# Optimization experiments

Measured on AMD Instinct MI355X. Metric: run time of the kernel, lower is better.

Reference implementation:

```python
import jax, jax.numpy as jnp
import numpy as np

M = 4        # num_modalities
C = 128      # in_channels
NH = 4       # num_heads
HD = C // NH # head_dim = 32
OUT = 128    # out_channels
B, D, H, W = 1, 12, 12, 12
N = D * H * W
EPS = 1e-5
SCALE = float(np.sqrt(HD))


def setup_inputs() -> dict:
    key = jax.random.key(0)
    ks = jax.random.split(key, 12)
    inp = {}
    for i in range(M):
        inp[f"feat{i}"] = jax.random.normal(ks[i], (B, C, D, H, W), dtype=jnp.float32)
    s = 1.0 / np.sqrt(C)
    inp["Wq"] = jax.random.normal(ks[4], (M, C, C), dtype=jnp.float32) * s
    inp["Wk"] = jax.random.normal(ks[5], (M, C, C), dtype=jnp.float32) * s
    inp["Wv"] = jax.random.normal(ks[6], (M, C, C), dtype=jnp.float32) * s
    inp["Wout"] = jax.random.normal(ks[7], (OUT, C), dtype=jnp.float32) * s
    inp["bn_gamma"] = jnp.ones((OUT,), jnp.float32)
    inp["bn_beta"] = jnp.zeros((OUT,), jnp.float32)
    inp["bn_mean"] = jax.random.normal(ks[8], (OUT,), dtype=jnp.float32) * 0.1
    inp["bn_var"] = jax.random.uniform(ks[9], (OUT,), dtype=jnp.float32, minval=0.5, maxval=1.5)
    return inp


def _proj(Wm, feats):
    # per-modality 1x1 conv == matmul over channels: [M,C,C] x [M,B,C,N] -> [M,B,nh,N,hd]
    p = jnp.einsum('moc,mbcn->mbon', Wm, feats)
    return p.reshape(M, B, NH, HD, N).transpose(0, 1, 2, 4, 3)


def reference(feat0, feat1, feat2, feat3, Wq, Wk, Wv, Wout,
              bn_gamma, bn_beta, bn_mean, bn_var):
    feats = jnp.stack([feat0, feat1, feat2, feat3]).reshape(M, B, C, N)
    Q = _proj(Wq, feats)   # [M,B,nh,N,hd]
    K = _proj(Wk, feats)
    V = _proj(Wv, feats)
    # concat K/V over modalities along token axis -> [B,nh,M*N,hd]
    Kall = K.transpose(1, 2, 0, 3, 4).reshape(B, NH, M * N, HD)
    Vall = V.transpose(1, 2, 0, 3, 4).reshape(B, NH, M * N, HD)
    fused = jnp.zeros((B, NH, N, HD), jnp.float32)
    for i in range(M):  # small fixed loop over modalities
        attn = jnp.einsum('bhqd,bhkd->bhqk', Q[i], Kall) / SCALE  # [B,nh,N,M*N]
        attn = jax.nn.softmax(attn, axis=-1)  # dropout is identity at eval
        fused = fused + jnp.einsum('bhqk,bhkd->bhqd', attn, Vall)
    fused = fused.transpose(0, 1, 3, 2).reshape(B, C, N)
    # out_proj: 1x1 Conv3d -> BN (eval, running stats) -> ReLU
    y = jnp.einsum('oc,bcn->bon', Wout, fused)
    inv = bn_gamma / jnp.sqrt(bn_var + EPS)
    y = y * inv[None, :, None] + (bn_beta - bn_mean * inv)[None, :, None]
    return jax.nn.relu(y).reshape(B, OUT, D, H, W)
```

## Files before the change

kernel.cpp:

```cpp
#include <hip/hip_runtime.h>

#define MODS 4
#define CH   128
#define NHD  4
#define HDIM 32
#define NTOK 1728
#define NG   (NTOK/4)
#define NKEY (MODS*NTOK)
#define NT   27
#define QSC (0.17677669529663687f * 1.4426950408889634f)

#ifndef __has_builtin
#define __has_builtin(x) 0
#endif
#if __has_builtin(__builtin_amdgcn_exp2f)
#define EXP2(x) __builtin_amdgcn_exp2f(x)
#else
#define EXP2(x) __expf(0.69314718055994531f * (x))
#endif

typedef __bf16 bf16x8 __attribute__((ext_vector_type(8)));
typedef float  f32x16 __attribute__((ext_vector_type(16)));

__device__ inline bf16x8 ldb8(const unsigned short* p) {
    return *reinterpret_cast<const bf16x8*>(p);
}
__device__ inline unsigned int pkbf(float a, float b) {
    unsigned short ua = __builtin_bit_cast(unsigned short, (__bf16)a);
    unsigned short ub = __builtin_bit_cast(unsigned short, (__bf16)b);
    return (unsigned int)ua | ((unsigned int)ub << 16);
}
__device__ inline void glds16(const unsigned short* g, unsigned short* l) {
    __builtin_amdgcn_global_load_lds(
        (const __attribute__((address_space(1))) unsigned int*)(g),
        (__attribute__((address_space(3))) unsigned int*)(l), 16, 0, 0);
}

__global__ __launch_bounds__(256) void proj_kernel(
    const float* __restrict__ f0, const float* __restrict__ f1,
    const float* __restrict__ f2, const float* __restrict__ f3,
    const float* __restrict__ Wq, const float* __restrict__ Wk,
    const float* __restrict__ Wv,
    unsigned short* __restrict__ Qb, unsigned short* __restrict__ Kb,
    unsigned short* __restrict__ V2)
{
    __shared__ __align__(16) float Wt[64][68];
    __shared__ __align__(16) float fs[64][68];

    const int tid = threadIdx.x;
    const int bid = blockIdx.x;
    const int tm  = bid / 54;
    const int rem = bid % 54;
    const int oh  = rem & 1;
    const int nt  = rem >> 1;
    const int t   = tm >> 2, m = tm & 3;
    const int nb  = nt * 64;

    const float* fsrc = (m == 0) ? f0 : (m == 1) ? f1 : (m == 2) ? f2 : f3;
    const float* W    = ((t == 0) ? Wq : (t == 1) ? Wk : Wv) + (size_t)m * CH * CH;

    const int o0 = (tid >> 4) * 4, nn0 = (tid & 15) * 4;
    float acc[4][4] = {};

    for (int ch = 0; ch < 2; ++ch) {
        if (ch) __syncthreads();
        {
            const int o = tid & 63, c4b = tid >> 6;
            #pragma unroll
            for (int j = 0; j < 4; ++j) {
                const int c4 = c4b + 4 * j;
                float4 wv = *reinterpret_cast<const float4*>(
                    W + (size_t)(oh * 64 + o) * CH + ch * 64 + c4 * 4);
                Wt[c4*4+0][o] = wv.x; Wt[c4*4+1][o] = wv.y;
                Wt[c4*4+2][o] = wv.z; Wt[c4*4+3][o] = wv.w;
            }
        }
        {
            const int nchunk = tid & 15, cb = tid >> 4;
            #pragma unroll
            for (int j = 0; j < 4; ++j) {
                const int c = cb + 16 * j;
                float4 v = *reinterpret_cast<const float4*>(
                    fsrc + (size_t)(ch * 64 + c) * NTOK + nb + nchunk * 4);
                *reinterpret_cast<float4*>(&fs[c][nchunk * 4]) = v;
            }
        }
        __syncthreads();
        #pragma unroll 4
        for (int c = 0; c < 64; ++c) {
            float4 wv = *reinterpret_cast<const float4*>(&Wt[c][o0]);
            float4 fv = *reinterpret_cast<const float4*>(&fs[c][nn0]);
            acc[0][0] = fmaf(wv.x, fv.x, acc[0][0]); acc[0][1] = fmaf(wv.x, fv.y, acc[0][1]);
            acc[0][2] = fmaf(wv.x, fv.z, acc[0][2]); acc[0][3] = fmaf(wv.x, fv.w, acc[0][3]);
            acc[1][0] = fmaf(wv.y, fv.x, acc[1][0]); acc[1][1] = fmaf(wv.y, fv.y, acc[1][1]);
            acc[1][2] = fmaf(wv.y, fv.z, acc[1][2]); acc[1][3] = fmaf(wv.y, fv.w, acc[1][3]);
            acc[2][0] = fmaf(wv.z, fv.x, acc[2][0]); acc[2][1] = fmaf(wv.z, fv.y, acc[2][1]);
            acc[2][2] = fmaf(wv.z, fv.z, acc[2][2]); acc[2][3] = fmaf(wv.z, fv.w, acc[2][3]);
            acc[3][0] = fmaf(wv.w, fv.x, acc[3][0]); acc[3][1] = fmaf(wv.w, fv.y, acc[3][1]);
            acc[3][2] = fmaf(wv.w, fv.z, acc[3][2]); acc[3][3] = fmaf(wv.w, fv.w, acc[3][3]);
        }
    }

    const int og0 = oh * 64 + o0;
    const int h = og0 >> 5, d0 = og0 & 31;
    const int ng = nb + nn0;
    if (t == 2) {
        const int off = ng & 15;
        const int ng2 = (ng & ~15) + ((off & 4) << 1) + ((off & 8) >> 1);
        #pragma unroll
        for (int i = 0; i < 4; ++i) {
            ushort4 pk;
            pk.x = __builtin_bit_cast(unsigned short, (__bf16)acc[i][0]);
            pk.y = __builtin_bit_cast(unsigned short, (__bf16)acc[i][1]);
            pk.z = __builtin_bit_cast(unsigned short, (__bf16)acc[i][2]);
            pk.w = __builtin_bit_cast(unsigned short, (__bf16)acc[i][3]);
            *reinterpret_cast<ushort4*>(V2 + (size_t)(h * HDIM + d0 + i) * NKEY + m * NTOK + ng2) = pk;
        }
    } else {
        const float sc = (t == 0) ? QSC : 1.0f;
        unsigned short* base = ((t == 0) ? Qb : Kb)
            + (((size_t)(m * NHD + h)) * NTOK + ng) * HDIM + d0;
        #pragma unroll
        for (int j = 0; j < 4; ++j) {
            unsigned short* row = base + (size_t)j * HDIM;
            *reinterpret_cast<unsigned int*>(row)     = pkbf(acc[0][j] * sc, acc[1][j] * sc);
            *reinterpret_cast<unsigned int*>(row + 2) = pkbf(acc[2][j] * sc, acc[3][j] * sc);
        }
    }
}

__global__ __launch_bounds__(256, 6) void attn_kernel(
    const unsigned short* __restrict__ Qb, const unsigned short* __restrict__ Kb,
    const unsigned short* __restrict__ V2,
    float* __restrict__ accT, float* __restrict__ sR)
{
    __shared__ __align__(16) unsigned short smAll[2][2][2][1024];

    const int tid  = threadIdx.x;
    const int lane = tid & 63;
    const int w    = tid >> 6;
    const int qslot = w & 1;
    const int ks    = w >> 1;
    const int l31  = lane & 31;
    const int hi   = lane >> 5;

    const int bid  = blockIdx.x;
    const int slot = bid & 7;
    const int h    = slot >> 1;
    const int ko   = slot & 1;
    const int rest = bid >> 3;
    const int qb   = rest % 108;
    const int kseg = rest / 108;
    const int qtile = qb * 2 + qslot;
    const int qg0  = qtile * 32;
    const int im   = qg0 / NTOK;
    const int n0   = qg0 % NTOK;
    const int km   = ko * 2 + ks;
    const int p    = kseg * 2 + ko;

    const unsigned short* qp = Qb + (((size_t)(im * NHD + h)) * NTOK + n0 + l31) * HDIM + hi * 8;
    const bf16x8 qf0 = ldb8(qp);
    const bf16x8 qf1 = ldb8(qp + 16);

    const int rk0 = qslot * 16 + (lane >> 2);
    const int ck0 = (lane & 3) ^ ((rk0 >> 1) & 3);
    const unsigned short* gk0 = Kb
        + (((size_t)(km * NHD + h)) * NTOK + kseg * 864 + rk0) * HDIM + ck0 * 8;
    const int dv0 = qslot * 16 + (lane >> 2);
    const int cv0 = (lane & 3) ^ (dv0 & 3);
    const unsigned short* gv0 = V2
        + ((size_t)(h * HDIM + dv0)) * NKEY + km * NTOK + kseg * 864 + cv0 * 8;

    const int fK = (l31 >> 1) & 3, fV = l31 & 3;
    const int kA0 = l31 * 32 + ((hi ^ fK) << 3);
    const int kB0 = l31 * 32 + (((2 + hi) ^ fK) << 3);
    const int vo0 = l31 * 32 + ((hi ^ fV) << 3);
    const int vo1 = l31 * 32 + (((2 + hi) ^ fV) << 3);

    f32x16 z;
    #pragma unroll
    for (int r = 0; r < 16; ++r) z[r] = 0.f;
    f32x16 o_acc = z, s_acc = z;
    bf16x8 onesv;
    #pragma unroll
    for (int j = 0; j < 8; ++j) onesv[j] = (__bf16)1.0f;

    #define STAGE(bb) do {                                      \
        glds16(gk0, &smAll[bb][ks][0][0] + qslot * 512);        \
        glds16(gv0, &smAll[bb][ks][1][0] + qslot * 512);        \
        gk0 += 1024; gv0 += 32;                                 \
    } while (0)

    STAGE(0);
    __syncthreads();

    int buf = 0;
    for (int t = 0; t < NT; ++t) {
        if (t + 1 < NT) STAGE(buf ^ 1);
        const unsigned short* Kl = &smAll[buf][ks][0][0];
        const unsigned short* Vl = &smAll[buf][ks][1][0];

        bf16x8 k0 = ldb8(Kl + kA0);
        bf16x8 k1 = ldb8(Kl + kB0);
        f32x16 c = __builtin_amdgcn_mfma_f32_32x32x16_bf16(k0, qf0, z, 0, 0, 0);
        c = __builtin_amdgcn_mfma_f32_32x32x16_bf16(k1, qf1, c, 0, 0, 0);

        float e[16];
        #pragma unroll
        for (int r = 0; r < 16; ++r) e[r] = EXP2(c[r]);
        bf16x8 pa0, pa1;
        #pragma unroll
        for (int j = 0; j < 8; ++j) { pa0[j] = (__bf16)e[j]; pa1[j] = (__bf16)e[8 + j]; }

        bf16x8 v0 = ldb8(Vl + vo0);
        bf16x8 v1 = ldb8(Vl + vo1);

        o_acc = __builtin_amdgcn_mfma_f32_32x32x16_bf16(pa0, v0, o_acc, 0, 0, 0);
        o_acc = __builtin_amdgcn_mfma_f32_32x32x16_bf16(pa1, v1, o_acc, 0, 0, 0);
        s_acc = __builtin_amdgcn_mfma_f32_32x32x16_bf16(pa0, onesv, s_acc, 0, 0, 0);
        s_acc = __builtin_amdgcn_mfma_f32_32x32x16_bf16(pa1, onesv, s_acc, 0, 0, 0);

        __syncthreads();
        buf ^= 1;
    }
    #undef STAGE

    float* accf = (float*)&smAll[0][0][0][0];
    if (ks == 1) {
        #pragma unroll
        for (int r = 0; r < 16; ++r) {
            const int qrow = (r & 3) + 8 * (r >> 2) + 4 * hi;
            accf[(qslot * 32 + qrow) * 33 + l31] = o_acc[r];
            if (l31 == 0) accf[(qslot * 32 + qrow) * 33 + 32] = s_acc[r];
        }
    }
    __syncthreads();
    if (ks == 0) {
        #pragma unroll
        for (int r = 0; r < 16; ++r) {
            const int qrow = (r & 3) + 8 * (r >> 2) + 4 * hi;
            accf[(qslot * 32 + qrow) * 33 + l31] += o_acc[r];
            if (l31 == 0) accf[(qslot * 32 + qrow) * 33 + 32] += s_acc[r];
        }
    }
    __syncthreads();
    {
        const int q  = tid & 63;
        const int dq = tid >> 6;
        #pragma unroll
        for (int j = 0; j < 8; ++j) {
            const int d = dq * 8 + j;
            accT[((size_t)((p * 4 + h) * HDIM + d)) * NKEY + (size_t)qb * 64 + q]
                = accf[q * 33 + d];
        }
        if (tid < 64)
            sR[((size_t)(p * 4 + h)) * NKEY + (size_t)qb * 64 + tid] = accf[tid * 33 + 32];
    }
}

__global__ __launch_bounds__(256) void norm_kernel(
    const float* __restrict__ accT, const float* __restrict__ sR,
    float* __restrict__ fused)
{
    const int idx = blockIdx.x * 256 + threadIdx.x;
    const int c = idx / NTOK;
    const int n = idx % NTOK;
    const int h = c >> 5, d = c & 31;
    float acc = 0.f;
    #pragma unroll
    for (int imq = 0; imq < MODS; ++imq) {
        const size_t q = (size_t)imq * NTOK + n;
        float s = 0.f, a = 0.f;
        #pragma unroll
        for (int pp = 0; pp < 4; ++pp) {
            s += sR[(size_t)(pp * 4 + h) * NKEY + q];
            a += accT[((size_t)((pp * 4 + h) * HDIM + d)) * NKEY + q];
        }
        acc = fmaf(a, 1.0f / s, acc);
    }
    fused[idx] = acc;
}

__global__ __launch_bounds__(256) void outproj_kernel(
    const float* __restrict__ fused, const float* __restrict__ Wout,
    const float* __restrict__ gamma, const float* __restrict__ beta,
    const float* __restrict__ mean,  const float* __restrict__ var,
    float* __restrict__ out)
{
    const int idx = blockIdx.x * 256 + threadIdx.x;
    const int n2 = idx % (NTOK / 2);
    const int o  = idx / (NTOK / 2);
    const float* W     = Wout + (size_t)o * CH;
    const float* fbase = fused + n2 * 2;
    float a0 = 0.f, a1 = 0.f;
    #pragma unroll 8
    for (int c = 0; c < CH; c += 4) {
        float4 w4 = *reinterpret_cast<const float4*>(W + c);
        float2 r0 = *reinterpret_cast<const float2*>(fbase + (size_t)(c + 0) * NTOK);
        float2 r1 = *reinterpret_cast<const float2*>(fbase + (size_t)(c + 1) * NTOK);
        float2 r2 = *reinterpret_cast<const float2*>(fbase + (size_t)(c + 2) * NTOK);
        float2 r3 = *reinterpret_cast<const float2*>(fbase + (size_t)(c + 3) * NTOK);
        a0 = fmaf(w4.x, r0.x, a0); a0 = fmaf(w4.y, r1.x, a0);
        a0 = fmaf(w4.z, r2.x, a0); a0 = fmaf(w4.w, r3.x, a0);
        a1 = fmaf(w4.x, r0.y, a1); a1 = fmaf(w4.y, r1.y, a1);
        a1 = fmaf(w4.z, r2.y, a1); a1 = fmaf(w4.w, r3.y, a1);
    }
    float inv = gamma[o] * rsqrtf(var[o] + 1e-5f);
    float sh  = fmaf(-mean[o], inv, beta[o]);
    float2 y;
    y.x = fmaxf(fmaf(a0, inv, sh), 0.f);
    y.y = fmaxf(fmaf(a1, inv, sh), 0.f);
    *reinterpret_cast<float2*>(out + (size_t)o * NTOK + n2 * 2) = y;
}

extern "C" void kernel_launch(void* const* d_in, const int* in_sizes, int n_in,
                              void* d_out, int out_size, void* d_ws, size_t ws_size,
                              hipStream_t stream)
{
    const float* f0    = (const float*)d_in[0];
    const float* f1    = (const float*)d_in[1];
    const float* f2    = (const float*)d_in[2];
    const float* f3    = (const float*)d_in[3];
    const float* Wq    = (const float*)d_in[4];
    const float* Wk    = (const float*)d_in[5];
    const float* Wv    = (const float*)d_in[6];
    const float* Wout  = (const float*)d_in[7];
    const float* gamma = (const float*)d_in[8];
    const float* beta  = (const float*)d_in[9];
    const float* mean  = (const float*)d_in[10];
    const float* var   = (const float*)d_in[11];
    float* out = (float*)d_out;

    const size_t QKV = (size_t)MODS * NHD * NTOK * HDIM;
    unsigned short* Qb = (unsigned short*)d_ws;
    unsigned short* Kb = Qb + QKV;
    unsigned short* V2 = Kb + QKV;
    float* accT  = (float*)(V2 + QKV);
    float* sR    = accT + (size_t)4 * NHD * HDIM * NKEY;
    float* fused = sR + (size_t)4 * NHD * NKEY;

    proj_kernel<<<648, 256, 0, stream>>>(f0, f1, f2, f3, Wq, Wk, Wv, Qb, Kb, V2);
    attn_kernel<<<1728, 256, 0, stream>>>(Qb, Kb, V2, accT, sR);
    norm_kernel<<<(CH * NTOK) / 256, 256, 0, stream>>>(accT, sR, fused);
    outproj_kernel<<<(CH * NTOK / 2) / 256, 256, 0, stream>>>(
        fused, Wout, gamma, beta, mean, var, out);
}
```

Baseline: 77.93 us.

## Use bf16 MFMA for QKV projection with a transposing bf16 prep kernel

Adds a prep kernel that converts features to bf16 in token-major layout and converts the Q/K/V weights to bf16, folding the query scale into Wq. The projection kernel then computes each 32-token by 128-output tile with 32x32x16 bf16 MFMA instructions instead of scalar fp32 FMAs. Results are staged through shared memory to write the Q/K and permuted V layouts. This cuts the projection's ALU cost, at the price of an extra kernel launch, extra workspace traffic, and bf16 rounding of the inputs.

```diff
diff --git a/kernel.cpp b/kernel.cpp
--- a/kernel.cpp
+++ b/kernel.cpp
@@ -5,7 +5,6 @@
 #define NHD  4
 #define HDIM 32
 #define NTOK 1728
-#define NG   (NTOK/4)
 #define NKEY (MODS*NTOK)
 #define NT   27
 #define QSC (0.17677669529663687f * 1.4426950408889634f)
@@ -25,10 +24,8 @@
 __device__ inline bf16x8 ldb8(const unsigned short* p) {
     return *reinterpret_cast<const bf16x8*>(p);
 }
-__device__ inline unsigned int pkbf(float a, float b) {
-    unsigned short ua = __builtin_bit_cast(unsigned short, (__bf16)a);
-    unsigned short ub = __builtin_bit_cast(unsigned short, (__bf16)b);
-    return (unsigned int)ua | ((unsigned int)ub << 16);
+__device__ inline unsigned short bfc(float x) {
+    return __builtin_bit_cast(unsigned short, (__bf16)x);
 }
 __device__ inline void glds16(const unsigned short* g, unsigned short* l) {
     __builtin_amdgcn_global_load_lds(
@@ -36,96 +33,125 @@
         (__attribute__((address_space(3))) unsigned int*)(l), 16, 0, 0);
 }
 
-__global__ __launch_bounds__(256) void proj_kernel(
+__global__ __launch_bounds__(256) void prep_kernel(
     const float* __restrict__ f0, const float* __restrict__ f1,
     const float* __restrict__ f2, const float* __restrict__ f3,
     const float* __restrict__ Wq, const float* __restrict__ Wk,
     const float* __restrict__ Wv,
+    unsigned short* __restrict__ fbT, unsigned short* __restrict__ Wb)
+{
+    const int tid = threadIdx.x;
+    const int bid = blockIdx.x;
+    if (bid < 216) {
+        __shared__ float tile[64][65];
+        const int m  = bid / 54;
+        const int r  = bid % 54;
+        const int cb = (r / 27) * 64;
+        const int nb = (r % 27) * 64;
+        const float* fsrc = (m == 0) ? f0 : (m == 1) ? f1 : (m == 2) ? f2 : f3;
+        const int n4 = tid & 15, cr = tid >> 4;
+        #pragma unroll
+        for (int j = 0; j < 4; ++j) {
+            const int c = cr + 16 * j;
+            float4 v = *reinterpret_cast<const float4*>(
+                fsrc + (size_t)(cb + c) * NTOK + nb + n4 * 4);
+            tile[c][n4*4+0] = v.x; tile[c][n4*4+1] = v.y;
+            tile[c][n4*4+2] = v.z; tile[c][n4*4+3] = v.w;
+        }
+        __syncthreads();
+        const int cq = tid & 15, nr0 = tid >> 4;
+        #pragma unroll
+        for (int j = 0; j < 4; ++j) {
+            const int nr = nr0 + 16 * j;
+            ushort4 pk;
+            pk.x = bfc(tile[cq*4+0][nr]); pk.y = bfc(tile[cq*4+1][nr]);
+            pk.z = bfc(tile[cq*4+2][nr]); pk.w = bfc(tile[cq*4+3][nr]);
+            *reinterpret_cast<ushort4*>(
+                fbT + ((size_t)m * NTOK + nb + nr) * CH + cb + cq * 4) = pk;
+        }
+    } else {
+        const int wb = bid - 216;
+        const size_t base = ((size_t)wb * 256 + tid) * 32;
+        #pragma unroll
+        for (int g = 0; g < 8; ++g) {
+            const size_t i = base + g * 4;
+            const int t = (int)(i >> 16);
+            const size_t off = i & 65535;
+            const float* W = (t == 0) ? Wq : (t == 1) ? Wk : Wv;
+            float4 v = *reinterpret_cast<const float4*>(W + off);
+            const float sc = (t == 0) ? QSC : 1.0f;
+            ushort4 pk;
+            pk.x = bfc(v.x * sc); pk.y = bfc(v.y * sc);
+            pk.z = bfc(v.z * sc); pk.w = bfc(v.w * sc);
+            *reinterpret_cast<ushort4*>(Wb + i) = pk;
+        }
+    }
+}
+
+__global__ __launch_bounds__(256) void proj_kernel(
+    const unsigned short* __restrict__ Wb, const unsigned short* __restrict__ fbT,
     unsigned short* __restrict__ Qb, unsigned short* __restrict__ Kb,
     unsigned short* __restrict__ V2)
 {
-    __shared__ __align__(16) float Wt[64][68];
-    __shared__ __align__(16) float fs[64][68];
+    __shared__ __align__(16) float accf[128 * 33];
 
     const int tid = threadIdx.x;
+    const int lane = tid & 63;
+    const int w    = tid >> 6;
+    const int l31  = lane & 31;
+    const int hi   = lane >> 5;
+
     const int bid = blockIdx.x;
     const int tm  = bid / 54;
-    const int rem = bid % 54;
-    const int oh  = rem & 1;
-    const int nt  = rem >> 1;
+    const int nb  = (bid % 54) * 32;
     const int t   = tm >> 2, m = tm & 3;
-    const int nb  = nt * 64;
-
-    const float* fsrc = (m == 0) ? f0 : (m == 1) ? f1 : (m == 2) ? f2 : f3;
-    const float* W    = ((t == 0) ? Wq : (t == 1) ? Wk : Wv) + (size_t)m * CH * CH;
-
-    const int o0 = (tid >> 4) * 4, nn0 = (tid & 15) * 4;
-    float acc[4][4] = {};
-
-    for (int ch = 0; ch < 2; ++ch) {
-        if (ch) __syncthreads();
-        {
-            const int o = tid & 63, c4b = tid >> 6;
-            #pragma unroll
-            for (int j = 0; j < 4; ++j) {
-                const int c4 = c4b + 4 * j;
-                float4 wv = *reinterpret_cast<const float4*>(
-                    W + (size_t)(oh * 64 + o) * CH + ch * 64 + c4 * 4);
-                Wt[c4*4+0][o] = wv.x; Wt[c4*4+1][o] = wv.y;
-                Wt[c4*4+2][o] = wv.z; Wt[c4*4+3][o] = wv.w;
-            }
-        }
-        {
-            const int nchunk = tid & 15, cb = tid >> 4;
-            #pragma unroll
-            for (int j = 0; j < 4; ++j) {
-                const int c = cb + 16 * j;
-                float4 v = *reinterpret_cast<const float4*>(
-                    fsrc + (size_t)(ch * 64 + c) * NTOK + nb + nchunk * 4);
-                *reinterpret_cast<float4*>(&fs[c][nchunk * 4]) = v;
-            }
-        }
-        __syncthreads();
-        #pragma unroll 4
-        for (int c = 0; c < 64; ++c) {
-            float4 wv = *reinterpret_cast<const float4*>(&Wt[c][o0]);
-            float4 fv = *reinterpret_cast<const float4*>(&fs[c][nn0]);
-            acc[0][0] = fmaf(wv.x, fv.x, acc[0][0]); acc[0][1] = fmaf(wv.x, fv.y, acc[0][1]);
-            acc[0][2] = fmaf(wv.x, fv.z, acc[0][2]); acc[0][3] = fmaf(wv.x, fv.w, acc[0][3]);
-            acc[1][0] = fmaf(wv.y, fv.x, acc[1][0]); acc[1][1] = fmaf(wv.y, fv.y, acc[1][1]);
-            acc[1][2] = fmaf(wv.y, fv.z, acc[1][2]); acc[1][3] = fmaf(wv.y, fv.w, acc[1][3]);
-            acc[2][0] = fmaf(wv.z, fv.x, acc[2][0]); acc[2][1] = fmaf(wv.z, fv.y, acc[2][1]);
-            acc[2][2] = fmaf(wv.z, fv.z, acc[2][2]); acc[2][3] = fmaf(wv.z, fv.w, acc[2][3]);
-            acc[3][0] = fmaf(wv.w, fv.x, acc[3][0]); acc[3][1] = fmaf(wv.w, fv.y, acc[3][1]);
-            acc[3][2] = fmaf(wv.w, fv.z, acc[3][2]); acc[3][3] = fmaf(wv.w, fv.w, acc[3][3]);
-        }
-    }
-
-    const int og0 = oh * 64 + o0;
-    const int h = og0 >> 5, d0 = og0 & 31;
-    const int ng = nb + nn0;
-    if (t == 2) {
-        const int off = ng & 15;
-        const int ng2 = (ng & ~15) + ((off & 4) << 1) + ((off & 8) >> 1);
-        #pragma unroll
-        for (int i = 0; i < 4; ++i) {
+
+    const unsigned short* Wrow = Wb + (((size_t)tm * CH) + w * 32 + l31) * CH + hi * 8;
+    const unsigned short* Frow = fbT + ((size_t)m * NTOK + nb + l31) * CH + hi * 8;
+
+    f32x16 acc;
+    #pragma unroll
+    for (int r = 0; r < 16; ++r) acc[r] = 0.f;
+    #pragma unroll
+    for (int cc = 0; cc < 8; ++cc) {
+        bf16x8 a = ldb8(Wrow + cc * 16);
+        bf16x8 b = ldb8(Frow + cc * 16);
+        acc = __builtin_amdgcn_mfma_f32_32x32x16_bf16(a, b, acc, 0, 0, 0);
+    }
+    #pragma unroll
+    for (int r = 0; r < 16; ++r) {
+        const int orow = w * 32 + (r & 3) + 8 * (r >> 2) + 4 * hi;
+        accf[orow * 33 + l31] = acc[r];
+    }
+    __syncthreads();
+
+    if (t < 2) {
+        unsigned short* dstb = (t == 0) ? Qb : Kb;
+        const int nl = tid >> 3, dp = (tid & 7) * 4;
+        #pragma unroll
+        for (int h = 0; h < 4; ++h) {
             ushort4 pk;
-            pk.x = __builtin_bit_cast(unsigned short, (__bf16)acc[i][0]);
-            pk.y = __builtin_bit_cast(unsigned short, (__bf16)acc[i][1]);
-            pk.z = __builtin_bit_cast(unsigned short, (__bf16)acc[i][2]);
-            pk.w = __builtin_bit_cast(unsigned short, (__bf16)acc[i][3]);
-            *reinterpret_cast<ushort4*>(V2 + (size_t)(h * HDIM + d0 + i) * NKEY + m * NTOK + ng2) = pk;
+            pk.x = bfc(accf[(h * 32 + dp + 0) * 33 + nl]);
+            pk.y = bfc(accf[(h * 32 + dp + 1) * 33 + nl]);
+            pk.z = bfc(accf[(h * 32 + dp + 2) * 33 + nl]);
+            pk.w = bfc(accf[(h * 32 + dp + 3) * 33 + nl]);
+            *reinterpret_cast<ushort4*>(
+                dstb + (((size_t)(m * NHD + h)) * NTOK + nb + nl) * HDIM + dp) = pk;
         }
     } else {
-        const float sc = (t == 0) ? QSC : 1.0f;
-        unsigned short* base = ((t == 0) ? Qb : Kb)
-            + (((size_t)(m * NHD + h)) * NTOK + ng) * HDIM + d0;
-        #pragma unroll
-        for (int j = 0; j < 4; ++j) {
-            unsigned short* row = base + (size_t)j * HDIM;
-            *reinterpret_cast<unsigned int*>(row)     = pkbf(acc[0][j] * sc, acc[1][j] * sc);
-            *reinterpret_cast<unsigned int*>(row + 2) = pkbf(acc[2][j] * sc, acc[3][j] * sc);
-        }
+        const int row = tid >> 1, half = tid & 1;
+        const int nw = half * 16;
+        unsigned short* dst = V2 + (size_t)row * NKEY + (size_t)m * NTOK + nb + nw;
+        const float* src = &accf[row * 33 + nw];
+        ushort4 p0, p1, p2, p3;
+        p0.x = bfc(src[0]);  p0.y = bfc(src[1]);  p0.z = bfc(src[2]);  p0.w = bfc(src[3]);
+        p1.x = bfc(src[8]);  p1.y = bfc(src[9]);  p1.z = bfc(src[10]); p1.w = bfc(src[11]);
+        p2.x = bfc(src[4]);  p2.y = bfc(src[5]);  p2.z = bfc(src[6]);  p2.w = bfc(src[7]);
+        p3.x = bfc(src[12]); p3.y = bfc(src[13]); p3.z = bfc(src[14]); p3.w = bfc(src[15]);
+        *reinterpret_cast<ushort4*>(dst + 0)  = p0;
+        *reinterpret_cast<ushort4*>(dst + 4)  = p1;
+        *reinterpret_cast<ushort4*>(dst + 8)  = p2;
+        *reinterpret_cast<ushort4*>(dst + 12) = p3;
     }
 }
 
@@ -225,13 +251,13 @@
     }
     #undef STAGE
 
-    float* accf = (float*)&smAll[0][0][0][0];
+    float* accfL = (float*)&smAll[0][0][0][0];
     if (ks == 1) {
         #pragma unroll
         for (int r = 0; r < 16; ++r) {
             const int qrow = (r & 3) + 8 * (r >> 2) + 4 * hi;
-            accf[(qslot * 32 + qrow) * 33 + l31] = o_acc[r];
-            if (l31 == 0) accf[(qslot * 32 + qrow) * 33 + 32] = s_acc[r];
+            accfL[(qslot * 32 + qrow) * 33 + l31] = o_acc[r];
+            if (l31 == 0) accfL[(qslot * 32 + qrow) * 33 + 32] = s_acc[r];
         }
     }
     __syncthreads();
@@ -239,8 +265,8 @@
         #pragma unroll
         for (int r = 0; r < 16; ++r) {
             const int qrow = (r & 3) + 8 * (r >> 2) + 4 * hi;
-            accf[(qslot * 32 + qrow) * 33 + l31] += o_acc[r];
-            if (l31 == 0) accf[(qslot * 32 + qrow) * 33 + 32] += s_acc[r];
+            accfL[(qslot * 32 + qrow) * 33 + l31] += o_acc[r];
+            if (l31 == 0) accfL[(qslot * 32 + qrow) * 33 + 32] += s_acc[r];
         }
     }
     __syncthreads();
@@ -251,10 +277,10 @@
         for (int j = 0; j < 8; ++j) {
             const int d = dq * 8 + j;
             accT[((size_t)((p * 4 + h) * HDIM + d)) * NKEY + (size_t)qb * 64 + q]
-                = accf[q * 33 + d];
+                = accfL[q * 33 + d];
         }
         if (tid < 64)
-            sR[((size_t)(p * 4 + h)) * NKEY + (size_t)qb * 64 + tid] = accf[tid * 33 + 32];
+            sR[((size_t)(p * 4 + h)) * NKEY + (size_t)qb * 64 + tid] = accfL[tid * 33 + 32];
     }
 }
 
@@ -332,14 +358,17 @@
     float* out = (float*)d_out;
 
     const size_t QKV = (size_t)MODS * NHD * NTOK * HDIM;
-    unsigned short* Qb = (unsigned short*)d_ws;
-    unsigned short* Kb = Qb + QKV;
-    unsigned short* V2 = Kb + QKV;
-    float* accT  = (float*)(V2 + QKV);
+    unsigned short* Qb  = (unsigned short*)d_ws;
+    unsigned short* Kb  = Qb + QKV;
+    unsigned short* V2  = Kb + QKV;
+    unsigned short* fbT = V2 + QKV;
+    unsigned short* Wb  = fbT + QKV;
+    float* accT  = (float*)(Wb + (size_t)3 * MODS * CH * CH);
     float* sR    = accT + (size_t)4 * NHD * HDIM * NKEY;
     float* fused = sR + (size_t)4 * NHD * NKEY;
 
-    proj_kernel<<<648, 256, 0, stream>>>(f0, f1, f2, f3, Wq, Wk, Wv, Qb, Kb, V2);
+    prep_kernel<<<240, 256, 0, stream>>>(f0, f1, f2, f3, Wq, Wk, Wv, fbT, Wb);
+    proj_kernel<<<648, 256, 0, stream>>>(Wb, fbT, Qb, Kb, V2);
     attn_kernel<<<1728, 256, 0, stream>>>(Qb, Kb, V2, accT, sR);
     norm_kernel<<<(CH * NTOK) / 256, 256, 0, stream>>>(accT, sR, fused);
     outproj_kernel<<<(CH * NTOK / 2) / 256, 256, 0, stream>>>(
```

Measured after the change: 76.45 us. Within noise of the previous version (-1.9%).
